# Performance work log

Hardware: AMD Instinct MI355X
Metric: run time of the kernel (lower is better)

## Reference

```python
import jax, jax.numpy as jnp
import numpy as np

B, C, H, W = 4, 96, 64, 64
CS = 8                      # chunk size
DN = 2 * C                  # d_inner (expand=2)
N = 16                      # d_state
K = 4                       # scan directions
DT_R = (C + 15) // 16       # dt_rank = ceil(d_model/16)
EPS = 1e-5


def _ln(x, g, b):
    m = x.mean(-1, keepdims=True)
    v = ((x - m) ** 2).mean(-1, keepdims=True)
    return (x - m) / jnp.sqrt(v + EPS) * g + b


def _selective_scan(xs, delta, A, Bs, Cs, D):
    # xs, delta: (Bc, K, Dn, L); Bs, Cs: (Bc, K, N, L); A: (K, Dn, N); D: (K, Dn)
    Bc, Kk, Dn, L = xs.shape
    uT = xs.transpose(3, 0, 1, 2)       # (L, Bc, K, Dn)
    dT = delta.transpose(3, 0, 1, 2)
    BT = Bs.transpose(3, 0, 1, 2)       # (L, Bc, K, N)
    CT = Cs.transpose(3, 0, 1, 2)

    def step(h, inp):
        u_l, d_l, B_l, C_l = inp
        dA = jnp.exp(d_l[..., None] * A)                       # (Bc,K,Dn,N)
        h = h * dA + (d_l * u_l)[..., None] * B_l[:, :, None, :]
        y = jnp.einsum('bkdn,bkn->bkd', h, C_l)
        return h, y

    h0 = jnp.zeros((Bc, Kk, Dn, A.shape[-1]), xs.dtype)
    _, ys = jax.lax.scan(step, h0, (uT, dT, BT, CT))           # ys: (L,Bc,K,Dn)
    ys = ys.transpose(1, 2, 3, 0)                              # (Bc,K,Dn,L)
    return ys + D[None, :, :, None] * xs


def _ss2d(xh, in_proj_w, conv_w, conv_b, x_proj_w, dt_w, dt_b,
          A_logs, Ds, outnorm_g, outnorm_b, out_proj_w):
    # xh: (Bc, Hc, Wc, C)
    Bc, Hc, Wc, _ = xh.shape
    L = Hc * Wc
    xz = xh @ in_proj_w                                        # (Bc,Hc,Wc,2*Dn)
    xc, z = jnp.split(xz, 2, axis=-1)
    xc = xc.transpose(0, 3, 1, 2)                              # (Bc,Dn,Hc,Wc)
    xc = jax.lax.conv_general_dilated(xc, conv_w, (1, 1), ((1, 1), (1, 1)),
                                      feature_group_count=DN)
    xc = jax.nn.silu(xc + conv_b[None, :, None, None])
    x0 = xc.reshape(Bc, DN, L)                                 # HW order
    x1 = xc.transpose(0, 1, 3, 2).reshape(Bc, DN, L)           # WH order
    xs = jnp.stack([x0, x1, x0[:, :, ::-1], x1[:, :, ::-1]], axis=1)  # (Bc,4,Dn,L)
    x_dbl = jnp.einsum('bkdl,kcd->bkcl', xs, x_proj_w)         # (Bc,4,DT_R+2N,L)
    dts = x_dbl[:, :, :DT_R]
    Bs = x_dbl[:, :, DT_R:DT_R + N]
    Cs = x_dbl[:, :, DT_R + N:]
    dts = jnp.einsum('bkrl,kdr->bkdl', dts, dt_w)
    delta = jax.nn.softplus(dts + dt_b[None, :, :, None])      # (Bc,4,Dn,L)
    A = -jnp.exp(A_logs).reshape(K, DN, N)
    ys = _selective_scan(xs, delta, A, Bs, Cs, Ds.reshape(K, DN))
    y0 = ys[:, 0]
    y1 = ys[:, 1].reshape(Bc, DN, Wc, Hc).transpose(0, 1, 3, 2).reshape(Bc, DN, L)
    y2 = ys[:, 2, :, ::-1]
    y3 = ys[:, 3, :, ::-1].reshape(Bc, DN, Wc, Hc).transpose(0, 1, 3, 2).reshape(Bc, DN, L)
    y = (y0 + y1 + y2 + y3).transpose(0, 2, 1)                 # (Bc,L,Dn)
    y = _ln(y, outnorm_g, outnorm_b).reshape(Bc, Hc, Wc, DN)
    y = y * jax.nn.silu(z)
    return y @ out_proj_w                                      # (Bc,Hc,Wc,C)


def reference(x, gamma, beta, alpha, ln1_g, ln1_b, in_proj_w, conv_w, conv_b,
              x_proj_w, dt_w, dt_b, A_logs, Ds, outnorm_g, outnorm_b, out_proj_w):
    Bb, Cc, Hh, Ww = x.shape
    # StateNorm: per (b, c) over spatial dims, unbiased=False
    mean = x.mean(axis=(2, 3), keepdims=True)
    var = ((x - mean) ** 2).mean(axis=(2, 3), keepdims=True)
    x_norm = (x - mean) / jnp.sqrt(var + EPS)
    x_norm = gamma[None, :, None, None] * x_norm + beta[None, :, None, None]
    x_act = jax.nn.silu(x_norm)                 # act_quant with bits=32 is identity
    hn, wn = Hh // CS, Ww // CS
    # chunk: b c (hn cs)(wn cs) -> (b hn wn) c cs cs
    xc = x_act.reshape(Bb, Cc, hn, CS, wn, CS).transpose(0, 2, 4, 1, 3, 5)
    xc = xc.reshape(Bb * hn * wn, Cc, CS, CS)
    # VSSBlock: h + SS2D(LN(h)) in BHWC (drop_path = identity at inference)
    h = xc.transpose(0, 2, 3, 1)                # (Bc, cs, cs, C)
    h = h + _ss2d(_ln(h, ln1_g, ln1_b), in_proj_w, conv_w, conv_b, x_proj_w,
                  dt_w, dt_b, A_logs, Ds, outnorm_g, outnorm_b, out_proj_w)
    xv = h.transpose(0, 3, 1, 2)                # back to BCHW
    # unchunk
    xv = xv.reshape(Bb, hn, wn, Cc, CS, CS).transpose(0, 3, 1, 4, 2, 5)
    xv = xv.reshape(Bb, Cc, Hh, Ww)
    return x + alpha * xv


def setup_inputs() -> dict:
    key = jax.random.key(0)
    ks = jax.random.split(key, 12)
    s = 0.02
    inp = {
        'x': jax.random.normal(ks[0], (B, C, H, W), jnp.float32),
        'gamma': jnp.ones((C,), jnp.float32),
        'beta': jnp.zeros((C,), jnp.float32),
        'alpha': jnp.float32(0.5),
        'ln1_g': jnp.ones((C,), jnp.float32),
        'ln1_b': jnp.zeros((C,), jnp.float32),
        'in_proj_w': jax.random.normal(ks[1], (C, 2 * DN), jnp.float32) / np.sqrt(C),
        'conv_w': jax.random.normal(ks[2], (DN, 1, 3, 3), jnp.float32) / 3.0,
        'conv_b': jnp.zeros((DN,), jnp.float32),
        'x_proj_w': jax.random.normal(ks[3], (K, DT_R + 2 * N, DN), jnp.float32) / np.sqrt(DN),
        'dt_w': jax.random.normal(ks[4], (K, DN, DT_R), jnp.float32) * (DT_R ** -0.5),
        'dt_b': jnp.full((K, DN), -4.6, jnp.float32) + s * jax.random.normal(ks[5], (K, DN), jnp.float32),
        'A_logs': jnp.log(jnp.broadcast_to(jnp.arange(1, N + 1, dtype=jnp.float32), (K * DN, N))).copy(),
        'Ds': jnp.ones((K * DN,), jnp.float32),
        'outnorm_g': jnp.ones((DN,), jnp.float32),
        'outnorm_b': jnp.zeros((DN,), jnp.float32),
        'out_proj_w': jax.random.normal(ks[6], (DN, C), jnp.float32) / np.sqrt(DN),
    }
    return inp
```

## Files before the change

kernel.cpp:

```cpp
#include <hip/hip_runtime.h>
#include <math.h>

#define NCHUNK 256
#define CCH    96
#define DNC    192
#define NST    16
#define DTR    6
#define PROW   48

__device__ __forceinline__ float siluf_(float x) {
    return x / (1.f + __expf(-x));
}

__device__ __forceinline__ int sperm(int k, int l) {
    int t = (k & 1) ? (((l & 7) << 3) | (l >> 3)) : l;
    return (k & 2) ? (63 - t) : t;
}

__global__ void k1a_stats(const float* __restrict__ x, float* __restrict__ stats) {
    int bc = blockIdx.x;
    const float* xp = x + (size_t)bc * 4096;
    float s = 0.f, sq = 0.f;
    for (int i = threadIdx.x; i < 4096; i += 256) {
        float v = xp[i]; s += v; sq += v * v;
    }
    __shared__ float rs[256], rq[256];
    rs[threadIdx.x] = s; rq[threadIdx.x] = sq;
    __syncthreads();
    for (int off = 128; off > 0; off >>= 1) {
        if (threadIdx.x < off) {
            rs[threadIdx.x] += rs[threadIdx.x + off];
            rq[threadIdx.x] += rq[threadIdx.x + off];
        }
        __syncthreads();
    }
    if (threadIdx.x == 0) {
        float m = rs[0] * (1.f / 4096.f);
        float v = rq[0] * (1.f / 4096.f) - m * m;
        stats[bc] = m;
        stats[384 + bc] = rsqrtf(v + 1e-5f);
    }
}

__global__ void ksetup(const float* __restrict__ xpw, float* __restrict__ wTg) {
    int k = blockIdx.x;
    for (int i = threadIdx.x; i < 192 * PROW; i += 256) {
        int dd = i / PROW, slot = i % PROW;
        int c = -1;
        if (slot < 6) c = slot;
        else if (slot >= 8 && slot < 40) c = slot - 2;
        float v = (c >= 0) ? xpw[((size_t)k * 38 + c) * 192 + dd] : 0.f;
        wTg[((size_t)k * 192 + dd) * PROW + slot] = v;
    }
}

__global__ __launch_bounds__(768, 1) void kfused(
        const float* __restrict__ x, const float* __restrict__ stats,
        const float* __restrict__ gamma, const float* __restrict__ beta,
        const float* __restrict__ ln1_g, const float* __restrict__ ln1_b,
        const float* __restrict__ Win,
        const float* __restrict__ conv_w, const float* __restrict__ conv_b,
        const float* __restrict__ wTg,
        const float* __restrict__ dtw, const float* __restrict__ dtb,
        const float* __restrict__ A_logs, const float* __restrict__ Ds,
        const float* __restrict__ og, const float* __restrict__ ob,
        const float* __restrict__ Wout,
        const float* __restrict__ alpha,
        float* __restrict__ zg_all,
        float* __restrict__ Pg_all,
        float* __restrict__ out) {
    __shared__ float hs[64][97];
    __shared__ float xln[64][97];
    __shared__ float xc[192][65];
    __shared__ float x0[192][65];

    int chunk = blockIdx.x;
    int t = threadIdx.x;
    int b = chunk >> 6, chh = (chunk >> 3) & 7, chw = chunk & 7;

    for (int i = t; i < 6144; i += 768) {
        int c = i >> 6, pos = i & 63;
        int bc = b * 96 + c;
        int hh = chh * 8 + (pos >> 3), ww = chw * 8 + (pos & 7);
        float v = x[(((size_t)bc) * 64 + hh) * 64 + ww];
        float xn = (v - stats[bc]) * stats[384 + bc] * gamma[c] + beta[c];
        hs[pos][c] = siluf_(xn);
    }
    __syncthreads();

    if (t < 512) {
        int p = t >> 3, o = t & 7;
        float s = 0.f, sq = 0.f;
        for (int j = 0; j < 12; j++) { float v = hs[p][o + 8 * j]; s += v; sq += v * v; }
        s += __shfl_xor(s, 1); sq += __shfl_xor(sq, 1);
        s += __shfl_xor(s, 2); sq += __shfl_xor(sq, 2);
        s += __shfl_xor(s, 4); sq += __shfl_xor(sq, 4);
        float m = s * (1.f / 96.f);
        float rinv = rsqrtf(sq * (1.f / 96.f) - m * m + 1e-5f);
        for (int j = 0; j < 12; j++) {
            int c = o + 8 * j;
            xln[p][c] = (hs[p][c] - m) * rinv * ln1_g[c] + ln1_b[c];
        }
    }
    __syncthreads();

    {
        int p = t & 63;
        int wv = __builtin_amdgcn_readfirstlane(t >> 6);
        int jbase = wv * 32;
        float acc[32];
        #pragma unroll
        for (int i = 0; i < 32; i++) acc[i] = 0.f;
        for (int c = 0; c < 96; c++) {
            float u = xln[p][c];
            const float* w = Win + c * 384 + jbase;
            #pragma unroll
            for (int i = 0; i < 32; i++) acc[i] = fmaf(u, w[i], acc[i]);
        }
        if (jbase < 192) {
            #pragma unroll
            for (int i = 0; i < 32; i++) xc[jbase + i][p] = acc[i];
        } else {
            float* zg = zg_all + (size_t)chunk * 12288 + (jbase - 192) * 64 + p;
            #pragma unroll
            for (int i = 0; i < 32; i++) zg[i * 64] = acc[i];
        }
    }
    __syncthreads();

    for (int s = 0; s < 16; s++) {
        int o = t + s * 768;
        int d = o >> 6, l = o & 63;
        int r = l >> 3, cc = l & 7;
        float acc = conv_b[d];
        #pragma unroll
        for (int dh = 0; dh < 3; dh++) {
            int rr = r + dh - 1;
            if (rr < 0 || rr > 7) continue;
            #pragma unroll
            for (int dw = 0; dw < 3; dw++) {
                int cw = cc + dw - 1;
                if (cw < 0 || cw > 7) continue;
                acc = fmaf(xc[d][rr * 8 + cw], conv_w[d * 9 + dh * 3 + dw], acc);
            }
        }
        x0[d][l] = siluf_(acc);
    }
    __syncthreads();

    {
        int k = __builtin_amdgcn_readfirstlane(t / 192);
        int tk = t - k * 192;
        int l = tk & 63;
        int cg = __builtin_amdgcn_readfirstlane(tk >> 6);
        int cbase = cg * 16;
        float acc[16];
        #pragma unroll
        for (int i = 0; i < 16; i++) acc[i] = 0.f;
        for (int dd = 0; dd < 192; dd++) {
            float u = x0[dd][l];
            const float* w = wTg + ((size_t)k * 192 + dd) * PROW + cbase;
            #pragma unroll
            for (int i = 0; i < 16; i++) acc[i] = fmaf(u, w[i], acc[i]);
        }
        float* pg = Pg_all + (size_t)(chunk * 4 + k) * 3072 + l * PROW + cbase;
        #pragma unroll
        for (int i = 0; i < 16; i += 4)
            *(float4*)(pg + i) = make_float4(acc[i], acc[i+1], acc[i+2], acc[i+3]);
    }
    for (int i = t; i < 12288; i += 768) {
        int d = i >> 6, l = i & 63;
        float dsum = Ds[d] + Ds[192 + d] + Ds[384 + d] + Ds[576 + d];
        xc[d][l] = dsum * x0[d][l];
    }
    __syncthreads();

    {
        int k = __builtin_amdgcn_readfirstlane(t / 192);
        int d = t - k * 192;
        int gd = k * 192 + d;
        float w6[6];
        #pragma unroll
        for (int r = 0; r < 6; r++) w6[r] = dtw[gd * 6 + r];
        float bias = dtb[gd];
        float a[16];
        #pragma unroll
        for (int n = 0; n < 16; n++) a[n] = -__expf(A_logs[gd * 16 + n]);
        bool pw = true;
        #pragma unroll
        for (int n = 1; n < 16; n++)
            pw = pw && (fabsf(a[n] - (float)(n + 1) * a[0]) <= 1e-4f * fabsf(a[n]) + 1e-6f);
        float hst[16];
        #pragma unroll
        for (int n = 0; n < 16; n++) hst[n] = 0.f;
        const float* pbase = Pg_all + (size_t)(chunk * 4 + k) * 3072;

        if (__all(pw)) {
            float a0 = a[0];
            for (int l = 0; l < 64; l++) {
                int sl = sperm(k, l);
                const float* row = pbase + sl * PROW;
                float u = x0[d][sl];
                float dp = bias;
                #pragma unroll
                for (int r = 0; r < 6; r++) dp = fmaf(row[r], w6[r], dp);
                float ex = __expf(dp);
                float delta = (dp > 20.f) ? dp : __logf(1.f + ex);
                float du = delta * u;
                float e1 = __expf(delta * a0);
                float p[16];
                p[0] = e1;
                p[1] = e1 * e1;
                p[2] = p[1] * e1;   p[3] = p[1] * p[1];
                p[4] = p[3] * e1;   p[5] = p[3] * p[1];
                p[6] = p[3] * p[2]; p[7] = p[3] * p[3];
                p[8] = p[7] * e1;   p[9] = p[7] * p[1];
                p[10] = p[7] * p[2]; p[11] = p[7] * p[3];
                p[12] = p[7] * p[4]; p[13] = p[7] * p[5];
                p[14] = p[7] * p[6]; p[15] = p[7] * p[7];
                float y0 = 0.f, y1 = 0.f, y2 = 0.f, y3 = 0.f;
                #pragma unroll
                for (int n = 0; n < 16; n += 4) {
                    hst[n]     = fmaf(hst[n],     p[n],     du * row[8 + n]);
                    hst[n + 1] = fmaf(hst[n + 1], p[n + 1], du * row[9 + n]);
                    hst[n + 2] = fmaf(hst[n + 2], p[n + 2], du * row[10 + n]);
                    hst[n + 3] = fmaf(hst[n + 3], p[n + 3], du * row[11 + n]);
                    y0 = fmaf(hst[n],     row[24 + n], y0);
                    y1 = fmaf(hst[n + 1], row[25 + n], y1);
                    y2 = fmaf(hst[n + 2], row[26 + n], y2);
                    y3 = fmaf(hst[n + 3], row[27 + n], y3);
                }
                atomicAdd(&xc[d][sl], (y0 + y1) + (y2 + y3));
            }
        } else {
            for (int l = 0; l < 64; l++) {
                int sl = sperm(k, l);
                const float* row = pbase + sl * PROW;
                float u = x0[d][sl];
                float dp = bias;
                #pragma unroll
                for (int r = 0; r < 6; r++) dp = fmaf(row[r], w6[r], dp);
                float ex = __expf(dp);
                float delta = (dp > 20.f) ? dp : __logf(1.f + ex);
                float du = delta * u;
                float y = 0.f;
                #pragma unroll
                for (int n = 0; n < 16; n++) {
                    float e = __expf(delta * a[n]);
                    hst[n] = fmaf(hst[n], e, du * row[8 + n]);
                    y = fmaf(hst[n], row[24 + n], y);
                }
                atomicAdd(&xc[d][sl], y);
            }
        }
    }
    __syncthreads();

    float* gbuf = &x0[0][0];
    if (t < 512) {
        int p = t >> 3, o = t & 7;
        float s = 0.f, sq = 0.f;
        for (int j = 0; j < 24; j++) { float v = xc[o + 8 * j][p]; s += v; sq += v * v; }
        s += __shfl_xor(s, 1); sq += __shfl_xor(sq, 1);
        s += __shfl_xor(s, 2); sq += __shfl_xor(sq, 2);
        s += __shfl_xor(s, 4); sq += __shfl_xor(sq, 4);
        float m = s * (1.f / 192.f);
        float rinv = rsqrtf(sq * (1.f / 192.f) - m * m + 1e-5f);
        const float* zg = zg_all + (size_t)chunk * 12288;
        for (int j = 0; j < 24; j++) {
            int i = o + 8 * j;
            float ln = (xc[i][p] - m) * rinv * og[i] + ob[i];
            float zv = zg[i * 64 + p];
            gbuf[p * 193 + i] = ln * siluf_(zv);
        }
    }
    __syncthreads();

    {
        int p = t & 63;
        int wv = __builtin_amdgcn_readfirstlane(t >> 6);
        int cbase = wv * 8;
        float acc[8];
        #pragma unroll
        for (int i = 0; i < 8; i++) acc[i] = 0.f;
        for (int dd = 0; dd < 192; dd++) {
            float u = gbuf[p * 193 + dd];
            const float* w = Wout + dd * 96 + cbase;
            #pragma unroll
            for (int i = 0; i < 8; i++) acc[i] = fmaf(u, w[i], acc[i]);
        }
        float al = alpha[0];
        int hh = chh * 8 + (p >> 3), ww = chw * 8 + (p & 7);
        #pragma unroll
        for (int i = 0; i < 8; i++) {
            int c = cbase + i;
            float hnew = hs[p][c] + acc[i];
            size_t gi = (((size_t)(b * 96 + c)) * 64 + hh) * 64 + ww;
            out[gi] = x[gi] + al * hnew;
        }
    }
}

extern "C" void kernel_launch(void* const* d_in, const int* in_sizes, int n_in,
                              void* d_out, int out_size, void* d_ws, size_t ws_size,
                              hipStream_t stream) {
    const float* x        = (const float*)d_in[0];
    const float* gamma    = (const float*)d_in[1];
    const float* beta     = (const float*)d_in[2];
    const float* alpha    = (const float*)d_in[3];
    const float* ln1_g    = (const float*)d_in[4];
    const float* ln1_b    = (const float*)d_in[5];
    const float* in_proj  = (const float*)d_in[6];
    const float* conv_w   = (const float*)d_in[7];
    const float* conv_b   = (const float*)d_in[8];
    const float* x_proj   = (const float*)d_in[9];
    const float* dt_w     = (const float*)d_in[10];
    const float* dt_b     = (const float*)d_in[11];
    const float* A_logs   = (const float*)d_in[12];
    const float* Ds       = (const float*)d_in[13];
    const float* onorm_g  = (const float*)d_in[14];
    const float* onorm_b  = (const float*)d_in[15];
    const float* out_proj = (const float*)d_in[16];
    float* out = (float*)d_out;

    float* ws   = (float*)d_ws;
    float* stats = ws;
    float* wTg   = ws + 768;
    float* zbuf  = wTg + 36864;
    float* Pg    = zbuf + 3145728;

    hipLaunchKernelGGL(k1a_stats, dim3(384), dim3(256), 0, stream, x, stats);
    hipLaunchKernelGGL(ksetup, dim3(4), dim3(256), 0, stream, x_proj, wTg);
    hipLaunchKernelGGL(kfused, dim3(256), dim3(768), 0, stream,
                       x, stats, gamma, beta, ln1_g, ln1_b, in_proj,
                       conv_w, conv_b, wTg, dt_w, dt_b, A_logs, Ds,
                       onorm_g, onorm_b, out_proj, alpha, zbuf, Pg, out);
}
```

Measured before the change: 217.9 us.

## Shrink fused kernel LDS to one arena by staging intermediates in global memory

Replaces the four shared-memory tiles with a single reused shared arena, so LDS use drops from roughly 150 KB to about 50 KB. The in-projection output, the conv output and the scan accumulation move to global workspace buffers, and the scan now does global atomicAdds. The residual silu(norm(x)) is recomputed in the epilogue instead of being kept in LDS. Launch bounds are raised to ask for higher occupancy. The cost is more global traffic and atomics, plus possible register pressure or spills from the tighter launch bounds. The grid is only 256 blocks, so extra occupancy may have little to act on.

```diff
diff --git a/kernel.cpp b/kernel.cpp
--- a/kernel.cpp
+++ b/kernel.cpp
@@ -54,7 +54,7 @@
     }
 }
 
-__global__ __launch_bounds__(768, 1) void kfused(
+__global__ __launch_bounds__(768, 6) void kfused(
         const float* __restrict__ x, const float* __restrict__ stats,
         const float* __restrict__ gamma, const float* __restrict__ beta,
         const float* __restrict__ ln1_g, const float* __restrict__ ln1_b,
@@ -66,13 +66,12 @@
         const float* __restrict__ og, const float* __restrict__ ob,
         const float* __restrict__ Wout,
         const float* __restrict__ alpha,
+        float* __restrict__ xcg_all,
         float* __restrict__ zg_all,
+        float* __restrict__ x0g_all,
         float* __restrict__ Pg_all,
         float* __restrict__ out) {
-    __shared__ float hs[64][97];
-    __shared__ float xln[64][97];
-    __shared__ float xc[192][65];
-    __shared__ float x0[192][65];
+    __shared__ float arena[12480];
 
     int chunk = blockIdx.x;
     int t = threadIdx.x;
@@ -84,14 +83,14 @@
         int hh = chh * 8 + (pos >> 3), ww = chw * 8 + (pos & 7);
         float v = x[(((size_t)bc) * 64 + hh) * 64 + ww];
         float xn = (v - stats[bc]) * stats[384 + bc] * gamma[c] + beta[c];
-        hs[pos][c] = siluf_(xn);
+        arena[pos * 97 + c] = siluf_(xn);
     }
     __syncthreads();
 
     if (t < 512) {
         int p = t >> 3, o = t & 7;
         float s = 0.f, sq = 0.f;
-        for (int j = 0; j < 12; j++) { float v = hs[p][o + 8 * j]; s += v; sq += v * v; }
+        for (int j = 0; j < 12; j++) { float v = arena[p * 97 + o + 8 * j]; s += v; sq += v * v; }
         s += __shfl_xor(s, 1); sq += __shfl_xor(sq, 1);
         s += __shfl_xor(s, 2); sq += __shfl_xor(sq, 2);
         s += __shfl_xor(s, 4); sq += __shfl_xor(sq, 4);
@@ -99,7 +98,7 @@
         float rinv = rsqrtf(sq * (1.f / 96.f) - m * m + 1e-5f);
         for (int j = 0; j < 12; j++) {
             int c = o + 8 * j;
-            xln[p][c] = (hs[p][c] - m) * rinv * ln1_g[c] + ln1_b[c];
+            arena[p * 97 + c] = (arena[p * 97 + c] - m) * rinv * ln1_g[c] + ln1_b[c];
         }
     }
     __syncthreads();
@@ -112,14 +111,15 @@
         #pragma unroll
         for (int i = 0; i < 32; i++) acc[i] = 0.f;
         for (int c = 0; c < 96; c++) {
-            float u = xln[p][c];
+            float u = arena[p * 97 + c];
             const float* w = Win + c * 384 + jbase;
             #pragma unroll
             for (int i = 0; i < 32; i++) acc[i] = fmaf(u, w[i], acc[i]);
         }
         if (jbase < 192) {
-            #pragma unroll
-            for (int i = 0; i < 32; i++) xc[jbase + i][p] = acc[i];
+            float* xg = xcg_all + (size_t)chunk * 12288 + jbase * 64 + p;
+            #pragma unroll
+            for (int i = 0; i < 32; i++) xg[i * 64] = acc[i];
         } else {
             float* zg = zg_all + (size_t)chunk * 12288 + (jbase - 192) * 64 + p;
             #pragma unroll
@@ -128,23 +128,29 @@
     }
     __syncthreads();
 
-    for (int s = 0; s < 16; s++) {
-        int o = t + s * 768;
-        int d = o >> 6, l = o & 63;
-        int r = l >> 3, cc = l & 7;
-        float acc = conv_b[d];
-        #pragma unroll
-        for (int dh = 0; dh < 3; dh++) {
-            int rr = r + dh - 1;
-            if (rr < 0 || rr > 7) continue;
-            #pragma unroll
-            for (int dw = 0; dw < 3; dw++) {
-                int cw = cc + dw - 1;
-                if (cw < 0 || cw > 7) continue;
-                acc = fmaf(xc[d][rr * 8 + cw], conv_w[d * 9 + dh * 3 + dw], acc);
+    {
+        const float* xg = xcg_all + (size_t)chunk * 12288;
+        float* x0g = x0g_all + (size_t)chunk * 12288;
+        for (int s = 0; s < 16; s++) {
+            int o = t + s * 768;
+            int d = o >> 6, l = o & 63;
+            int r = l >> 3, cc = l & 7;
+            float acc = conv_b[d];
+            #pragma unroll
+            for (int dh = 0; dh < 3; dh++) {
+                int rr = r + dh - 1;
+                if (rr < 0 || rr > 7) continue;
+                #pragma unroll
+                for (int dw = 0; dw < 3; dw++) {
+                    int cw = cc + dw - 1;
+                    if (cw < 0 || cw > 7) continue;
+                    acc = fmaf(xg[d * 64 + rr * 8 + cw], conv_w[d * 9 + dh * 3 + dw], acc);
+                }
             }
-        }
-        x0[d][l] = siluf_(acc);
+            float v = siluf_(acc);
+            arena[d * 65 + l] = v;
+            x0g[o] = v;
+        }
     }
     __syncthreads();
 
@@ -158,7 +164,7 @@
         #pragma unroll
         for (int i = 0; i < 16; i++) acc[i] = 0.f;
         for (int dd = 0; dd < 192; dd++) {
-            float u = x0[dd][l];
+            float u = arena[dd * 65 + l];
             const float* w = wTg + ((size_t)k * 192 + dd) * PROW + cbase;
             #pragma unroll
             for (int i = 0; i < 16; i++) acc[i] = fmaf(u, w[i], acc[i]);
@@ -168,10 +174,9 @@
         for (int i = 0; i < 16; i += 4)
             *(float4*)(pg + i) = make_float4(acc[i], acc[i+1], acc[i+2], acc[i+3]);
     }
-    for (int i = t; i < 12288; i += 768) {
-        int d = i >> 6, l = i & 63;
-        float dsum = Ds[d] + Ds[192 + d] + Ds[384 + d] + Ds[576 + d];
-        xc[d][l] = dsum * x0[d][l];
+    {
+        float* yac = xcg_all + (size_t)chunk * 12288;
+        for (int i = t; i < 12288; i += 768) yac[i] = 0.f;
     }
     __syncthreads();
 
@@ -179,6 +184,7 @@
         int k = __builtin_amdgcn_readfirstlane(t / 192);
         int d = t - k * 192;
         int gd = k * 192 + d;
+        float* yac = xcg_all + (size_t)chunk * 12288;
         float w6[6];
         #pragma unroll
         for (int r = 0; r < 6; r++) w6[r] = dtw[gd * 6 + r];
@@ -200,7 +206,7 @@
             for (int l = 0; l < 64; l++) {
                 int sl = sperm(k, l);
                 const float* row = pbase + sl * PROW;
-                float u = x0[d][sl];
+                float u = arena[d * 65 + sl];
                 float dp = bias;
                 #pragma unroll
                 for (int r = 0; r < 6; r++) dp = fmaf(row[r], w6[r], dp);
@@ -230,13 +236,13 @@
                     y2 = fmaf(hst[n + 2], row[26 + n], y2);
                     y3 = fmaf(hst[n + 3], row[27 + n], y3);
                 }
-                atomicAdd(&xc[d][sl], (y0 + y1) + (y2 + y3));
+                atomicAdd(&yac[sl * 192 + d], (y0 + y1) + (y2 + y3));
             }
         } else {
             for (int l = 0; l < 64; l++) {
                 int sl = sperm(k, l);
                 const float* row = pbase + sl * PROW;
-                float u = x0[d][sl];
+                float u = arena[d * 65 + sl];
                 float dp = bias;
                 #pragma unroll
                 for (int r = 0; r < 6; r++) dp = fmaf(row[r], w6[r], dp);
@@ -250,28 +256,37 @@
                     hst[n] = fmaf(hst[n], e, du * row[8 + n]);
                     y = fmaf(hst[n], row[24 + n], y);
                 }
-                atomicAdd(&xc[d][sl], y);
+                atomicAdd(&yac[sl * 192 + d], y);
             }
         }
     }
     __syncthreads();
 
-    float* gbuf = &x0[0][0];
     if (t < 512) {
         int p = t >> 3, o = t & 7;
+        const float* yac = xcg_all + (size_t)chunk * 12288;
+        const float* x0g = x0g_all + (size_t)chunk * 12288;
+        const float* zg  = zg_all  + (size_t)chunk * 12288;
+        float ys[24];
         float s = 0.f, sq = 0.f;
-        for (int j = 0; j < 24; j++) { float v = xc[o + 8 * j][p]; s += v; sq += v * v; }
+        #pragma unroll
+        for (int j = 0; j < 24; j++) {
+            int i = o + 8 * j;
+            float dsum = Ds[i] + Ds[192 + i] + Ds[384 + i] + Ds[576 + i];
+            float v = yac[p * 192 + i] + dsum * x0g[i * 64 + p];
+            ys[j] = v;
+            s += v; sq += v * v;
+        }
         s += __shfl_xor(s, 1); sq += __shfl_xor(sq, 1);
         s += __shfl_xor(s, 2); sq += __shfl_xor(sq, 2);
         s += __shfl_xor(s, 4); sq += __shfl_xor(sq, 4);
         float m = s * (1.f / 192.f);
         float rinv = rsqrtf(sq * (1.f / 192.f) - m * m + 1e-5f);
-        const float* zg = zg_all + (size_t)chunk * 12288;
+        #pragma unroll
         for (int j = 0; j < 24; j++) {
             int i = o + 8 * j;
-            float ln = (xc[i][p] - m) * rinv * og[i] + ob[i];
-            float zv = zg[i * 64 + p];
-            gbuf[p * 193 + i] = ln * siluf_(zv);
+            float ln = (ys[j] - m) * rinv * og[i] + ob[i];
+            arena[p * 193 + i] = ln * siluf_(zg[i * 64 + p]);
         }
     }
     __syncthreads();
@@ -284,7 +299,7 @@
         #pragma unroll
         for (int i = 0; i < 8; i++) acc[i] = 0.f;
         for (int dd = 0; dd < 192; dd++) {
-            float u = gbuf[p * 193 + dd];
+            float u = arena[p * 193 + dd];
             const float* w = Wout + dd * 96 + cbase;
             #pragma unroll
             for (int i = 0; i < 8; i++) acc[i] = fmaf(u, w[i], acc[i]);
@@ -294,9 +309,13 @@
         #pragma unroll
         for (int i = 0; i < 8; i++) {
             int c = cbase + i;
-            float hnew = hs[p][c] + acc[i];
-            size_t gi = (((size_t)(b * 96 + c)) * 64 + hh) * 64 + ww;
-            out[gi] = x[gi] + al * hnew;
+            int bc = b * 96 + c;
+            size_t gi = (((size_t)bc) * 64 + hh) * 64 + ww;
+            float xv = x[gi];
+            float xn = (xv - stats[bc]) * stats[384 + bc] * gamma[c] + beta[c];
+            float hval = siluf_(xn);
+            float hnew = hval + acc[i];
+            out[gi] = xv + al * hnew;
         }
     }
 }
@@ -323,16 +342,19 @@
     const float* out_proj = (const float*)d_in[16];
     float* out = (float*)d_out;
 
-    float* ws   = (float*)d_ws;
+    float* ws    = (float*)d_ws;
     float* stats = ws;
     float* wTg   = ws + 768;
-    float* zbuf  = wTg + 36864;
-    float* Pg    = zbuf + 3145728;
+    float* xcg   = wTg + 36864;
+    float* zg    = xcg + 3145728;
+    float* x0g   = zg + 3145728;
+    float* Pg    = x0g + 3145728;
 
     hipLaunchKernelGGL(k1a_stats, dim3(384), dim3(256), 0, stream, x, stats);
     hipLaunchKernelGGL(ksetup, dim3(4), dim3(256), 0, stream, x_proj, wTg);
     hipLaunchKernelGGL(kfused, dim3(256), dim3(768), 0, stream,
                        x, stats, gamma, beta, ln1_g, ln1_b, in_proj,
                        conv_w, conv_b, wTg, dt_w, dt_b, A_logs, Ds,
-                       onorm_g, onorm_b, out_proj, alpha, zbuf, Pg, out);
-}
+                       onorm_g, onorm_b, out_proj, alpha,
+                       xcg, zg, x0g, Pg, out);
+}
```

Measured after the change: 228.2 us. 4.7% more time.
